# Performance work log

Hardware: AMD Instinct MI355X
Metric: run time of the kernel (lower is better)

The kernel has to match this reference:

```python
import jax, jax.numpy as jnp
import numpy as np

DS = 32   # self_obs_dim
DO = 32   # obstacle_obs_dim
D = DS + DO
H = 128   # obstacle_hidden_size
B = 512   # batch_size
A = 16    # num_adv_obs = 2 * num_oppo_obs


def _init_linear(key, fan_in, fan_out):
    kw, kb = jax.random.split(key)
    bound = 1.0 / np.sqrt(fan_in)
    w = jax.random.uniform(kw, (fan_in, fan_out), jnp.float32, -bound, bound)
    b = jax.random.uniform(kb, (fan_out,), jnp.float32, -bound, bound)
    return w, b


def setup_inputs() -> dict:
    key = jax.random.key(0)
    ks = jax.random.split(key, 10)
    obs = jax.random.normal(ks[0], (B, DS), jnp.float32)
    latent = jax.random.normal(ks[1], (B, A, DO), jnp.float32)
    hw1, hb1 = _init_linear(ks[2], D, H)
    hw2, hb2 = _init_linear(ks[3], H, D * H)
    vw1, vb1 = _init_linear(ks[4], H, H)
    vw2, vb2 = _init_linear(ks[5], H, H)
    aw1, ab1 = _init_linear(ks[6], 2 * H, H)
    aw2, ab2 = _init_linear(ks[7], H, H)
    aw3, ab3 = _init_linear(ks[8], H, 1)
    return {
        "obs": obs, "obs_intention_latent": latent,
        "hw1": hw1, "hb1": hb1, "hw2": hw2, "hb2": hb2,
        "vw1": vw1, "vb1": vb1, "vw2": vw2, "vb2": vb2,
        "aw1": aw1, "ab1": ab1, "aw2": aw2, "ab2": ab2,
        "aw3": aw3, "ab3": ab3,
        "num_adv_obs": A, "batch_size": B, "num_groups": 1,
    }


def reference(obs, obs_intention_latent, hw1, hb1, hw2, hb2,
              vw1, vb1, vw2, vb2, aw1, ab1, aw2, ab2, aw3, ab3,
              num_adv_obs, batch_size, num_groups):
    relu = jax.nn.relu
    # flatten opponents (batch-major, matches torch .reshape)
    obs_obstacles = obs_intention_latent.reshape(-1, DO)          # [N, DO]
    # torch .repeat(num_adv_obs, 1) tiles the batch dim
    self_rep = jnp.tile(obs[:, :DS], (num_adv_obs, 1))            # [N, DS]
    mlp_input = jnp.concatenate([self_rep, obs_obstacles], axis=1)  # [N, D]
    # hypernet: per-sample weight [N, D, H]
    h = relu(mlp_input @ hw1 + hb1)
    w = relu(h @ hw2 + hb2).reshape(-1, D, H)
    # per-sample vector-matrix product + tanh
    emb = jnp.tanh(jnp.einsum("nd,ndh->nh", mlp_input, w))        # [N, H]
    # neighbor value MLP
    vals = relu(relu(emb @ vw1 + vb1) @ vw2 + vb2)                # [N, H]
    # attention: concat with per-batch mean embedding
    emb_mean = jnp.mean(emb.reshape(batch_size, -1, H), axis=1)   # [B, H]
    mean_rep = jnp.tile(emb_mean, (num_adv_obs, 1))               # [N, H]
    att_in = jnp.concatenate([emb, mean_rep], axis=1)             # [N, 2H]
    scores = relu(relu(att_in @ aw1 + ab1) @ aw2 + ab2) @ aw3 + ab3  # [N, 1]
    att = jax.nn.softmax(scores.reshape(batch_size, -1), axis=1).reshape(-1, 1)
    weighted = (att * vals).reshape(batch_size, -1, H)
    return jnp.sum(weighted, axis=1)                              # [B, H]
```

## Files before the change

kernel.cpp:

```cpp
#include <hip/hip_runtime.h>
#include <hip/hip_bf16.h>
#include <math.h>

#define BATCH 512
#define NADV  16
#define NROWS (BATCH*NADV)
#define DS    32
#define DO    32
#define DIM   64
#define HID   128
#define WCOLS (DIM*HID)
#define LSTR  136
#define PACK_BLOCKS 276

typedef _Float16 half8 __attribute__((ext_vector_type(8)));
typedef float floatx4 __attribute__((ext_vector_type(4)));

__device__ inline void async_ld16(void* lds, const void* g) {
    __builtin_amdgcn_global_load_lds(
        (const __attribute__((address_space(1))) void*)g,
        (__attribute__((address_space(3))) void*)lds, 16, 0, 0);
}

__global__ __launch_bounds__(256)
void k_prep(const float* __restrict__ obs, const float* __restrict__ latent,
            const float* __restrict__ hw1, const float* __restrict__ hb1,
            const float* __restrict__ hw2, const float* __restrict__ vw1,
            const float* __restrict__ vw2, const float* __restrict__ aw1,
            const float* __restrict__ aw2,
            _Float16* __restrict__ hf,
            _Float16* __restrict__ w2p, _Float16* __restrict__ vw1p,
            _Float16* __restrict__ vw2p, _Float16* __restrict__ aw1p,
            _Float16* __restrict__ aw2p) {
    __shared__ __align__(16) float smem[32 * 132];
    int b = blockIdx.x;
    int tid = threadIdx.x;
    if (b < PACK_BLOCKS) {
        const float* src; _Float16* dst; int N, Kt, jb, kt;
        if (b < 256)      { src = hw2; dst = w2p;  N = WCOLS; Kt = 4; jb = b >> 2; kt = b & 3; }
        else if (b < 260) { src = vw1; dst = vw1p; N = HID;   Kt = 4; jb = 0; kt = b - 256; }
        else if (b < 264) { src = vw2; dst = vw2p; N = HID;   Kt = 4; jb = 0; kt = b - 260; }
        else if (b < 272) { src = aw1; dst = aw1p; N = HID;   Kt = 8; jb = 0; kt = b - 264; }
        else              { src = aw2; dst = aw2p; N = HID;   Kt = 4; jb = 0; kt = b - 272; }
        for (int i = tid; i < 32 * 32; i += 256) {
            int r = i >> 5, c4 = (i & 31) * 4;
            *(float4*)&smem[r * 132 + c4] =
                *(const float4*)(src + (size_t)(kt * 32 + r) * N + jb * 128 + c4);
        }
        __syncthreads();
        for (int i = tid; i < 8 * 64; i += 256) {
            int ctl = i >> 6, lane = i & 63;
            int ct = jb * 8 + ctl;
            int rbase = (lane >> 4) * 8, cc = ctl * 16 + (lane & 15);
            half8 v;
#pragma unroll
            for (int e = 0; e < 8; ++e) v[e] = (_Float16)smem[(rbase + e) * 132 + cc];
            *(half8*)(dst + ((size_t)ct * Kt + kt) * 512 + lane * 8) = v;
        }
    } else {
        int n0 = (b - PACK_BLOCKS) * 16;
        int wave = tid >> 6, lane = tid & 63, l15 = lane & 15, quad = lane >> 4;
        half8 af2[2];
        {
            int n = n0 + l15;
            const float* orow = obs + (size_t)(n & (BATCH - 1)) * DS + quad * 8;
            const float* lrow = latent + (size_t)n * DO + quad * 8;
            float4 a0 = *(const float4*)orow;
            float4 a1 = *(const float4*)(orow + 4);
            float4 c0 = *(const float4*)lrow;
            float4 c1 = *(const float4*)(lrow + 4);
            float a8[8] = {a0.x, a0.y, a0.z, a0.w, a1.x, a1.y, a1.z, a1.w};
            float c8[8] = {c0.x, c0.y, c0.z, c0.w, c1.x, c1.y, c1.z, c1.w};
#pragma unroll
            for (int e = 0; e < 8; ++e) {
                af2[0][e] = (_Float16)a8[e];
                af2[1][e] = (_Float16)c8[e];
            }
        }
#pragma unroll
        for (int cti = 0; cti < 2; ++cti) {
            int ct = wave * 2 + cti;
            float bb = hb1[ct * 16 + l15];
            floatx4 acc = {bb, bb, bb, bb};
#pragma unroll
            for (int ks = 0; ks < 2; ++ks) {
                const float* wsrc = hw1 + (size_t)(ks * 32 + quad * 8) * HID + ct * 16 + l15;
                half8 bf;
#pragma unroll
                for (int e = 0; e < 8; ++e) bf[e] = (_Float16)wsrc[e * HID];
                acc = __builtin_amdgcn_mfma_f32_16x16x32_f16(af2[ks], bf, acc, 0, 0, 0);
            }
#pragma unroll
            for (int reg = 0; reg < 4; ++reg)
                hf[(size_t)(n0 + quad * 4 + reg) * HID + ct * 16 + l15] =
                    (_Float16)fmaxf(acc[reg], 0.f);
        }
    }
}

__global__ __launch_bounds__(256, 2)
void k_hyper_mfma(const float* __restrict__ obs, const float* __restrict__ latent,
                  const _Float16* __restrict__ hf, const _Float16* __restrict__ w2p,
                  const float* __restrict__ hb2,
                  _Float16* __restrict__ embf, _Float16* __restrict__ emeanf) {
    __shared__ __align__(16) _Float16 Bs[8][4][512];
    __shared__ __align__(16) float xs_t[64][132];
    __shared__ float bias_s[64 * 16];
    int b  = blockIdx.x;
    int jt = b & 7;
    int rt = b >> 3;
    int n0 = rt * 128;
    int j0 = jt * 16;
    int tid = threadIdx.x;
    int wave = tid >> 6, lane = tid & 63;
    int l15 = lane & 15, quad = lane >> 4;

    for (int i = tid; i < 128 * 16; i += 256) {
        int r = i >> 4, c4 = (i & 15) * 4;
        float4 v;
        if (c4 < DS) v = *(const float4*)(obs + ((n0 + r) & (BATCH - 1)) * DS + c4);
        else         v = *(const float4*)(latent + (size_t)(n0 + r) * DO + (c4 - DS));
        xs_t[c4 + 0][r] = v.x;
        xs_t[c4 + 1][r] = v.y;
        xs_t[c4 + 2][r] = v.z;
        xs_t[c4 + 3][r] = v.w;
    }
    for (int i = tid; i < 64 * 16; i += 256)
        bias_s[i] = hb2[(i >> 4) * HID + j0 + (i & 15)];

    half8 af[2][4];
#pragma unroll
    for (int t = 0; t < 2; ++t) {
        const _Float16* arow = hf + (size_t)(n0 + wave * 32 + t * 16 + l15) * HID;
#pragma unroll
        for (int ks = 0; ks < 4; ++ks)
            af[t][ks] = *(const half8*)(arow + ks * 32 + quad * 8);
    }

    float emb_acc[2][4] = {{0.f, 0.f, 0.f, 0.f}, {0.f, 0.f, 0.f, 0.f}};

    for (int d8 = 0; d8 < 8; ++d8) {
#pragma unroll
        for (int s = 0; s < 2; ++s) {
            int dt = wave * 2 + s;
            int ct = (d8 * 8 + dt) * 8 + jt;
            const _Float16* src = w2p + (size_t)ct * 2048 + lane * 8;
            _Float16* dst = &Bs[dt][0][0];
#pragma unroll
            for (int kt = 0; kt < 4; ++kt)
                async_ld16(dst + kt * 512, src + kt * 512);
        }
        __syncthreads();

#pragma unroll
        for (int dd = 0; dd < 8; ++dd) {
            int d = d8 * 8 + dd;
            float bb = bias_s[d * 16 + l15];
            floatx4 acc0 = {bb, bb, bb, bb};
            floatx4 acc1 = {bb, bb, bb, bb};
#pragma unroll
            for (int ks = 0; ks < 4; ++ks) {
                half8 bfr = *(const half8*)&Bs[dd][ks][lane * 8];
                acc0 = __builtin_amdgcn_mfma_f32_16x16x32_f16(af[0][ks], bfr, acc0, 0, 0, 0);
                acc1 = __builtin_amdgcn_mfma_f32_16x16x32_f16(af[1][ks], bfr, acc1, 0, 0, 0);
            }
            floatx4 xv0 = *(const floatx4*)&xs_t[d][wave * 32 + quad * 4];
            floatx4 xv1 = *(const floatx4*)&xs_t[d][wave * 32 + 16 + quad * 4];
#pragma unroll
            for (int reg = 0; reg < 4; ++reg) {
                emb_acc[0][reg] = fmaf(xv0[reg], fmaxf(acc0[reg], 0.f), emb_acc[0][reg]);
                emb_acc[1][reg] = fmaf(xv1[reg], fmaxf(acc1[reg], 0.f), emb_acc[1][reg]);
            }
        }
        __syncthreads();
    }

#pragma unroll
    for (int t = 0; t < 2; ++t) {
        float e[4];
#pragma unroll
        for (int reg = 0; reg < 4; ++reg) {
            e[reg] = tanhf(emb_acc[t][reg]);
            embf[(size_t)(n0 + wave * 32 + t * 16 + quad * 4 + reg) * HID + j0 + l15] =
                (_Float16)e[reg];
        }
        float s = e[0] + e[1] + e[2] + e[3];
        s += __shfl_xor(s, 16, 64);
        s += __shfl_xor(s, 32, 64);
        if (quad == 0)
            emeanf[(size_t)(rt * 8 + wave * 2 + t) * HID + j0 + l15] =
                (_Float16)(s * (1.f / 16));
    }
}

__global__ __launch_bounds__(512, 4)
void k_tail(const _Float16* __restrict__ embf, const _Float16* __restrict__ emeanf,
            const _Float16* __restrict__ vw1p, const float* __restrict__ vb1,
            const _Float16* __restrict__ vw2p, const float* __restrict__ vb2,
            const _Float16* __restrict__ aw1p, const float* __restrict__ ab1,
            const _Float16* __restrict__ aw2p, const float* __restrict__ ab2,
            const float* __restrict__ aw3, const float* __restrict__ ab3,
            float* __restrict__ out) {
    __shared__ _Float16 embs[16][LSTR];
    __shared__ _Float16 means[16][LSTR];
    __shared__ _Float16 tAs[16][LSTR];
    __shared__ _Float16 tBs[16][LSTR];
    __shared__ float scr[16][32];
    __shared__ float satt[16];
    __shared__ float att[16];
    int g = blockIdx.x;
    int n0 = g * 16;
    int tid = threadIdx.x;
    int wave = tid >> 6, lane = tid & 63, l15 = lane & 15, quad = lane >> 4;
    int ct = wave;

    {
        int m = tid >> 8, r = (tid >> 4) & 15, c8 = (tid & 15) * 8;
        if (m == 0)
            *(half8*)&embs[r][c8] = *(const half8*)(embf + (size_t)(n0 + r) * HID + c8);
        else
            *(half8*)&means[r][c8] =
                *(const half8*)(emeanf + (size_t)((n0 & 511) + r) * HID + c8);
    }
    __syncthreads();

    half8 av[4], amean[4];
#pragma unroll
    for (int ks = 0; ks < 4; ++ks) {
        av[ks]    = *(const half8*)&embs[l15][ks * 32 + quad * 8];
        amean[ks] = *(const half8*)&means[l15][ks * 32 + quad * 8];
    }

    floatx4 acc;
    {
        float bb = vb1[ct * 16 + l15];
        acc = (floatx4){bb, bb, bb, bb};
    }
#pragma unroll
    for (int ks = 0; ks < 4; ++ks) {
        half8 bfr = *(const half8*)(vw1p + ((size_t)ct * 4 + ks) * 512 + lane * 8);
        acc = __builtin_amdgcn_mfma_f32_16x16x32_f16(av[ks], bfr, acc, 0, 0, 0);
    }
#pragma unroll
    for (int reg = 0; reg < 4; ++reg)
        tAs[quad * 4 + reg][ct * 16 + l15] = (_Float16)fmaxf(acc[reg], 0.f);
    __syncthreads();

    half8 at[4];
#pragma unroll
    for (int ks = 0; ks < 4; ++ks)
        at[ks] = *(const half8*)&tAs[l15][ks * 32 + quad * 8];

    floatx4 vacc;
    {
        float bb = vb2[ct * 16 + l15];
        vacc = (floatx4){bb, bb, bb, bb};
    }
#pragma unroll
    for (int ks = 0; ks < 4; ++ks) {
        half8 bfr = *(const half8*)(vw2p + ((size_t)ct * 4 + ks) * 512 + lane * 8);
        vacc = __builtin_amdgcn_mfma_f32_16x16x32_f16(at[ks], bfr, vacc, 0, 0, 0);
    }

    floatx4 aacc;
    {
        float bb = ab1[ct * 16 + l15];
        aacc = (floatx4){bb, bb, bb, bb};
    }
#pragma unroll
    for (int ks = 0; ks < 8; ++ks) {
        half8 bfr = *(const half8*)(aw1p + ((size_t)ct * 8 + ks) * 512 + lane * 8);
        half8 a = (ks < 4) ? av[ks] : amean[ks - 4];
        aacc = __builtin_amdgcn_mfma_f32_16x16x32_f16(a, bfr, aacc, 0, 0, 0);
    }
#pragma unroll
    for (int reg = 0; reg < 4; ++reg)
        tBs[quad * 4 + reg][ct * 16 + l15] = (_Float16)fmaxf(aacc[reg], 0.f);
    __syncthreads();

    half8 aa[4];
#pragma unroll
    for (int ks = 0; ks < 4; ++ks)
        aa[ks] = *(const half8*)&tBs[l15][ks * 32 + quad * 8];

    floatx4 a2acc;
    {
        float bb = ab2[ct * 16 + l15];
        a2acc = (floatx4){bb, bb, bb, bb};
    }
#pragma unroll
    for (int ks = 0; ks < 4; ++ks) {
        half8 bfr = *(const half8*)(aw2p + ((size_t)ct * 4 + ks) * 512 + lane * 8);
        a2acc = __builtin_amdgcn_mfma_f32_16x16x32_f16(aa[ks], bfr, a2acc, 0, 0, 0);
    }
    __syncthreads();
#pragma unroll
    for (int reg = 0; reg < 4; ++reg)
        tAs[quad * 4 + reg][ct * 16 + l15] = (_Float16)fmaxf(a2acc[reg], 0.f);
    __syncthreads();

    {
        int r = tid >> 5, ch = tid & 31;
        float p = 0.f;
#pragma unroll
        for (int k = 0; k < 4; ++k)
            p += (float)tAs[r][ch * 4 + k] * aw3[ch * 4 + k];
        scr[r][ch] = p;
    }
    __syncthreads();
    if (tid < 16) {
        float s = ab3[0];
#pragma unroll
        for (int ch = 0; ch < 32; ++ch) s += scr[tid][ch];
        satt[tid] = s;
    }
    __syncthreads();
    if (tid < 16) {
        float m = -1e30f;
#pragma unroll
        for (int a = 0; a < 16; ++a) m = fmaxf(m, satt[a]);
        float S = 0.f;
#pragma unroll
        for (int a = 0; a < 16; ++a) S += expf(satt[a] - m);
        att[tid] = expf(satt[tid] - m) / S;
    }
    __syncthreads();

    {
        float p = 0.f;
#pragma unroll
        for (int reg = 0; reg < 4; ++reg)
            p += att[quad * 4 + reg] * fmaxf(vacc[reg], 0.f);
        p += __shfl_xor(p, 16, 64);
        p += __shfl_xor(p, 32, 64);
        if (quad == 0) out[(size_t)g * HID + ct * 16 + l15] = p;
    }
}

extern "C" void kernel_launch(void* const* d_in, const int* in_sizes, int n_in,
                              void* d_out, int out_size, void* d_ws, size_t ws_size,
                              hipStream_t stream) {
    const float* obs = (const float*)d_in[0];
    const float* lat = (const float*)d_in[1];
    const float* hw1 = (const float*)d_in[2];
    const float* hb1 = (const float*)d_in[3];
    const float* hw2 = (const float*)d_in[4];
    const float* hb2 = (const float*)d_in[5];
    const float* vw1 = (const float*)d_in[6];
    const float* vb1 = (const float*)d_in[7];
    const float* vw2 = (const float*)d_in[8];
    const float* vb2 = (const float*)d_in[9];
    const float* aw1 = (const float*)d_in[10];
    const float* ab1 = (const float*)d_in[11];
    const float* aw2 = (const float*)d_in[12];
    const float* ab2 = (const float*)d_in[13];
    const float* aw3 = (const float*)d_in[14];
    const float* ab3 = (const float*)d_in[15];
    float* out = (float*)d_out;

    char* ws = (char*)d_ws;
    _Float16*  hf     = (_Float16*)ws;  ws += (size_t)NROWS * HID * 2;
    _Float16*  w2p    = (_Float16*)ws;  ws += (size_t)WCOLS * HID * 2;
    _Float16*  embf   = (_Float16*)ws;  ws += (size_t)NROWS * HID * 2;
    _Float16*  emeanf = (_Float16*)ws;  ws += (size_t)BATCH * HID * 2;
    _Float16*  vw1p   = (_Float16*)ws;  ws += (size_t)HID * HID * 2;
    _Float16*  vw2p   = (_Float16*)ws;  ws += (size_t)HID * HID * 2;
    _Float16*  aw1p   = (_Float16*)ws;  ws += (size_t)2 * HID * HID * 2;
    _Float16*  aw2p   = (_Float16*)ws;  ws += (size_t)HID * HID * 2;

    hipLaunchKernelGGL(k_prep, dim3(PACK_BLOCKS + NROWS / 16), dim3(256), 0, stream,
                       obs, lat, hw1, hb1, hw2, vw1, vw2, aw1, aw2,
                       hf, w2p, vw1p, vw2p, aw1p, aw2p);
    hipLaunchKernelGGL(k_hyper_mfma, dim3(512), dim3(256), 0, stream,
                       obs, lat, hf, w2p, hb2, embf, emeanf);
    hipLaunchKernelGGL(k_tail, dim3(BATCH), dim3(512), 0, stream,
                       embf, emeanf, vw1p, vb1, vw2p, vb2,
                       aw1p, ab1, aw2p, ab2, aw3, ab3, out);
}
```

Baseline: 128.0 us.

## Split d across waves with per-wave triple-buffered async loads and LDS reduction

The hypernet GEMM kernel is restructured so each wave owns all 128 rows and a quarter of the d dimension. Each wave streams its own weight tiles through a 3-deep per-wave LDS ring using async global-to-LDS loads and explicit vmcnt waits, which replaces the block-wide __syncthreads per d-chunk. The four waves' partial embedding sums are then combined through LDS before tanh and the mean. The x tile is XOR-swizzled to reduce bank conflicts. The cost is 32 A fragments held per lane, which raises register pressure, plus the extra reduction pass.

Result: slower. 132.0 us (+3.1%).

```diff
diff --git a/kernel.cpp b/kernel.cpp
--- a/kernel.cpp
+++ b/kernel.cpp
@@ -21,6 +21,8 @@
         (const __attribute__((address_space(1))) void*)g,
         (__attribute__((address_space(3))) void*)lds, 16, 0, 0);
 }
+
+#define XSW(c) ((((c) >> 2) & 7) << 2)
 
 __global__ __launch_bounds__(256)
 void k_prep(const float* __restrict__ obs, const float* __restrict__ latent,
@@ -49,13 +51,13 @@
         }
         __syncthreads();
         for (int i = tid; i < 8 * 64; i += 256) {
-            int ctl = i >> 6, lane = i & 63;
+            int ctl = i >> 6, ln = i & 63;
             int ct = jb * 8 + ctl;
-            int rbase = (lane >> 4) * 8, cc = ctl * 16 + (lane & 15);
+            int rbase = (ln >> 4) * 8, cc = ctl * 16 + (ln & 15);
             half8 v;
 #pragma unroll
             for (int e = 0; e < 8; ++e) v[e] = (_Float16)smem[(rbase + e) * 132 + cc];
-            *(half8*)(dst + ((size_t)ct * Kt + kt) * 512 + lane * 8) = v;
+            *(half8*)(dst + ((size_t)ct * Kt + kt) * 512 + ln * 8) = v;
         }
     } else {
         int n0 = (b - PACK_BLOCKS) * 16;
@@ -65,16 +67,10 @@
             int n = n0 + l15;
             const float* orow = obs + (size_t)(n & (BATCH - 1)) * DS + quad * 8;
             const float* lrow = latent + (size_t)n * DO + quad * 8;
-            float4 a0 = *(const float4*)orow;
-            float4 a1 = *(const float4*)(orow + 4);
-            float4 c0 = *(const float4*)lrow;
-            float4 c1 = *(const float4*)(lrow + 4);
-            float a8[8] = {a0.x, a0.y, a0.z, a0.w, a1.x, a1.y, a1.z, a1.w};
-            float c8[8] = {c0.x, c0.y, c0.z, c0.w, c1.x, c1.y, c1.z, c1.w};
 #pragma unroll
             for (int e = 0; e < 8; ++e) {
-                af2[0][e] = (_Float16)a8[e];
-                af2[1][e] = (_Float16)c8[e];
+                af2[0][e] = (_Float16)orow[e];
+                af2[1][e] = (_Float16)lrow[e];
             }
         }
 #pragma unroll
@@ -87,7 +83,7 @@
                 const float* wsrc = hw1 + (size_t)(ks * 32 + quad * 8) * HID + ct * 16 + l15;
                 half8 bf;
 #pragma unroll
-                for (int e = 0; e < 8; ++e) bf[e] = (_Float16)wsrc[e * HID];
+                for (int e = 0; e < 8; ++e) bf[e] = (_Float16)wsrc[(size_t)e * HID];
                 acc = __builtin_amdgcn_mfma_f32_16x16x32_f16(af2[ks], bf, acc, 0, 0, 0);
             }
 #pragma unroll
@@ -99,97 +95,133 @@
 }
 
 __global__ __launch_bounds__(256, 2)
-void k_hyper_mfma(const float* __restrict__ obs, const float* __restrict__ latent,
-                  const _Float16* __restrict__ hf, const _Float16* __restrict__ w2p,
-                  const float* __restrict__ hb2,
-                  _Float16* __restrict__ embf, _Float16* __restrict__ emeanf) {
-    __shared__ __align__(16) _Float16 Bs[8][4][512];
-    __shared__ __align__(16) float xs_t[64][132];
-    __shared__ float bias_s[64 * 16];
-    int b  = blockIdx.x;
+void k_gemm(const float* __restrict__ obs, const float* __restrict__ latent,
+            const _Float16* __restrict__ hf, const _Float16* __restrict__ w2p,
+            const float* __restrict__ hb2,
+            _Float16* __restrict__ embf, _Float16* __restrict__ emeanf) {
+    __shared__ __align__(16) char smraw[81920];
+    float (*xs_t)[128] = (float(*)[128])smraw;
+    _Float16 (*Bs)[3][2048] = (_Float16(*)[3][2048])(smraw + 32768);
+
+    int b   = blockIdx.x;
+    int tid = threadIdx.x;
+    int wave = tid >> 6, lane = tid & 63, l15 = lane & 15, quad = lane >> 4;
+
     int jt = b & 7;
     int rt = b >> 3;
     int n0 = rt * 128;
     int j0 = jt * 16;
-    int tid = threadIdx.x;
-    int wave = tid >> 6, lane = tid & 63;
-    int l15 = lane & 15, quad = lane >> 4;
 
     for (int i = tid; i < 128 * 16; i += 256) {
         int r = i >> 4, c4 = (i & 15) * 4;
         float4 v;
         if (c4 < DS) v = *(const float4*)(obs + ((n0 + r) & (BATCH - 1)) * DS + c4);
         else         v = *(const float4*)(latent + (size_t)(n0 + r) * DO + (c4 - DS));
-        xs_t[c4 + 0][r] = v.x;
-        xs_t[c4 + 1][r] = v.y;
-        xs_t[c4 + 2][r] = v.z;
-        xs_t[c4 + 3][r] = v.w;
-    }
-    for (int i = tid; i < 64 * 16; i += 256)
-        bias_s[i] = hb2[(i >> 4) * HID + j0 + (i & 15)];
-
-    half8 af[2][4];
-#pragma unroll
-    for (int t = 0; t < 2; ++t) {
-        const _Float16* arow = hf + (size_t)(n0 + wave * 32 + t * 16 + l15) * HID;
+        xs_t[c4 + 0][r ^ XSW(c4 + 0)] = v.x;
+        xs_t[c4 + 1][r ^ XSW(c4 + 1)] = v.y;
+        xs_t[c4 + 2][r ^ XSW(c4 + 2)] = v.z;
+        xs_t[c4 + 3][r ^ XSW(c4 + 3)] = v.w;
+    }
+
+    half8 af[8][4];
+#pragma unroll
+    for (int t = 0; t < 8; ++t)
 #pragma unroll
         for (int ks = 0; ks < 4; ++ks)
-            af[t][ks] = *(const half8*)(arow + ks * 32 + quad * 8);
-    }
-
-    float emb_acc[2][4] = {{0.f, 0.f, 0.f, 0.f}, {0.f, 0.f, 0.f, 0.f}};
-
-    for (int d8 = 0; d8 < 8; ++d8) {
-#pragma unroll
-        for (int s = 0; s < 2; ++s) {
-            int dt = wave * 2 + s;
-            int ct = (d8 * 8 + dt) * 8 + jt;
-            const _Float16* src = w2p + (size_t)ct * 2048 + lane * 8;
-            _Float16* dst = &Bs[dt][0][0];
+            af[t][ks] = *(const half8*)(hf + (size_t)(n0 + t * 16 + l15) * HID
+                                           + ks * 32 + quad * 8);
+
+    float bias_r[16];
+#pragma unroll
+    for (int i = 0; i < 16; ++i) {
+        int d = (i >> 1) * 8 + wave * 2 + (i & 1);
+        bias_r[i] = hb2[d * HID + j0 + l15];
+    }
+
+    const _Float16* wbase = w2p + (size_t)jt * 2048 + lane * 8;
+#pragma unroll
+    for (int p = 0; p < 3; ++p) {
+        int d = (p >> 1) * 8 + wave * 2 + (p & 1);
+        const _Float16* src = wbase + (size_t)d * 16384;
+        _Float16* dst = &Bs[wave][p][0];
+#pragma unroll
+        for (int kt = 0; kt < 4; ++kt)
+            async_ld16(dst + kt * 512, src + kt * 512);
+    }
+    __syncthreads();
+
+    float emb_acc[8][4];
+#pragma unroll
+    for (int t = 0; t < 8; ++t)
+#pragma unroll
+        for (int reg = 0; reg < 4; ++reg) emb_acc[t][reg] = 0.f;
+
+#pragma unroll
+    for (int i = 0; i < 16; ++i) {
+        if (i <= 13)      asm volatile("s_waitcnt vmcnt(8)" ::: "memory");
+        else if (i == 14) asm volatile("s_waitcnt vmcnt(4)" ::: "memory");
+        else              asm volatile("s_waitcnt vmcnt(0)" ::: "memory");
+        __builtin_amdgcn_sched_barrier(0);
+
+        int d = (i >> 1) * 8 + wave * 2 + (i & 1);
+        int buf = i % 3;
+        half8 bfr0 = *(const half8*)&Bs[wave][buf][0 * 512 + lane * 8];
+        half8 bfr1 = *(const half8*)&Bs[wave][buf][1 * 512 + lane * 8];
+        half8 bfr2 = *(const half8*)&Bs[wave][buf][2 * 512 + lane * 8];
+        half8 bfr3 = *(const half8*)&Bs[wave][buf][3 * 512 + lane * 8];
+        float bb = bias_r[i];
+        int rsw = XSW(d);
+
+        __builtin_amdgcn_s_setprio(1);
+#pragma unroll
+        for (int t = 0; t < 8; ++t) {
+            floatx4 acc = {bb, bb, bb, bb};
+            acc = __builtin_amdgcn_mfma_f32_16x16x32_f16(af[t][0], bfr0, acc, 0, 0, 0);
+            acc = __builtin_amdgcn_mfma_f32_16x16x32_f16(af[t][1], bfr1, acc, 0, 0, 0);
+            acc = __builtin_amdgcn_mfma_f32_16x16x32_f16(af[t][2], bfr2, acc, 0, 0, 0);
+            acc = __builtin_amdgcn_mfma_f32_16x16x32_f16(af[t][3], bfr3, acc, 0, 0, 0);
+            floatx4 xv = *(const floatx4*)&xs_t[d][(t * 16 + quad * 4) ^ rsw];
+#pragma unroll
+            for (int reg = 0; reg < 4; ++reg)
+                emb_acc[t][reg] = fmaf(xv[reg], fmaxf(acc[reg], 0.f), emb_acc[t][reg]);
+        }
+        __builtin_amdgcn_s_setprio(0);
+
+        if (i + 3 < 16) {
+            int dn = ((i + 3) >> 1) * 8 + wave * 2 + ((i + 3) & 1);
+            const _Float16* src = wbase + (size_t)dn * 16384;
+            _Float16* dst = &Bs[wave][buf][0];
 #pragma unroll
             for (int kt = 0; kt < 4; ++kt)
                 async_ld16(dst + kt * 512, src + kt * 512);
         }
-        __syncthreads();
-
-#pragma unroll
-        for (int dd = 0; dd < 8; ++dd) {
-            int d = d8 * 8 + dd;
-            float bb = bias_s[d * 16 + l15];
-            floatx4 acc0 = {bb, bb, bb, bb};
-            floatx4 acc1 = {bb, bb, bb, bb};
-#pragma unroll
-            for (int ks = 0; ks < 4; ++ks) {
-                half8 bfr = *(const half8*)&Bs[dd][ks][lane * 8];
-                acc0 = __builtin_amdgcn_mfma_f32_16x16x32_f16(af[0][ks], bfr, acc0, 0, 0, 0);
-                acc1 = __builtin_amdgcn_mfma_f32_16x16x32_f16(af[1][ks], bfr, acc1, 0, 0, 0);
-            }
-            floatx4 xv0 = *(const floatx4*)&xs_t[d][wave * 32 + quad * 4];
-            floatx4 xv1 = *(const floatx4*)&xs_t[d][wave * 32 + 16 + quad * 4];
-#pragma unroll
-            for (int reg = 0; reg < 4; ++reg) {
-                emb_acc[0][reg] = fmaf(xv0[reg], fmaxf(acc0[reg], 0.f), emb_acc[0][reg]);
-                emb_acc[1][reg] = fmaf(xv1[reg], fmaxf(acc1[reg], 0.f), emb_acc[1][reg]);
-            }
-        }
-        __syncthreads();
-    }
-
-#pragma unroll
-    for (int t = 0; t < 2; ++t) {
+    }
+    __syncthreads();
+
+    float* red = (float*)smraw;
+#pragma unroll
+    for (int t = 0; t < 8; ++t)
+#pragma unroll
+        for (int reg = 0; reg < 4; ++reg)
+            red[((wave * 128) + t * 16 + quad * 4 + reg) * 16 + l15] = emb_acc[t][reg];
+    __syncthreads();
+#pragma unroll
+    for (int t2 = 0; t2 < 2; ++t2) {
         float e[4];
 #pragma unroll
-        for (int reg = 0; reg < 4; ++reg) {
-            e[reg] = tanhf(emb_acc[t][reg]);
-            embf[(size_t)(n0 + wave * 32 + t * 16 + quad * 4 + reg) * HID + j0 + l15] =
-                (_Float16)e[reg];
-        }
-        float s = e[0] + e[1] + e[2] + e[3];
-        s += __shfl_xor(s, 16, 64);
-        s += __shfl_xor(s, 32, 64);
+        for (int rr = 0; rr < 4; ++rr) {
+            int row = wave * 32 + t2 * 16 + quad * 4 + rr;
+            float s = red[(0 * 128 + row) * 16 + l15] + red[(1 * 128 + row) * 16 + l15]
+                    + red[(2 * 128 + row) * 16 + l15] + red[(3 * 128 + row) * 16 + l15];
+            e[rr] = tanhf(s);
+            embf[(size_t)(n0 + row) * HID + j0 + l15] = (_Float16)e[rr];
+        }
+        float m = e[0] + e[1] + e[2] + e[3];
+        m += __shfl_xor(m, 16, 64);
+        m += __shfl_xor(m, 32, 64);
         if (quad == 0)
-            emeanf[(size_t)(rt * 8 + wave * 2 + t) * HID + j0 + l15] =
-                (_Float16)(s * (1.f / 16));
+            emeanf[(size_t)(rt * 8 + wave * 2 + t2) * HID + j0 + l15] =
+                (_Float16)(m * (1.f / 16));
     }
 }
 
@@ -371,7 +403,7 @@
     hipLaunchKernelGGL(k_prep, dim3(PACK_BLOCKS + NROWS / 16), dim3(256), 0, stream,
                        obs, lat, hw1, hb1, hw2, vw1, vw2, aw1, aw2,
                        hf, w2p, vw1p, vw2p, aw1p, aw2p);
-    hipLaunchKernelGGL(k_hyper_mfma, dim3(512), dim3(256), 0, stream,
+    hipLaunchKernelGGL(k_gemm, dim3(512), dim3(256), 0, stream,
                        obs, lat, hf, w2p, hb2, embf, emeanf);
     hipLaunchKernelGGL(k_tail, dim3(BATCH), dim3(512), 0, stream,
                        embf, emeanf, vw1p, vb1, vw2p, vb2,
```
